# Optimization experiments

Hardware: AMD Instinct MI355X
Metric: run time of the kernel (lower is better)

Reference implementation:

```python
import jax, jax.numpy as jnp
import numpy as np

FEATURE_DIM = 512
DEPTH = 128
NUM_CLASSES = 1000


def setup_inputs() -> dict:
    key = jax.random.key(0)
    ks = jax.random.split(key, 9)
    s = 1.0 / np.sqrt(FEATURE_DIM)
    sd = 1.0 / np.sqrt(DEPTH)
    return {
        "x": jax.random.normal(ks[0], (8, 2048, FEATURE_DIM), dtype=jnp.float32),
        "Wq": jax.random.uniform(ks[1], (FEATURE_DIM, DEPTH), jnp.float32, -s, s),
        "bq": jax.random.uniform(ks[2], (DEPTH,), jnp.float32, -s, s),
        "Wk": jax.random.uniform(ks[3], (FEATURE_DIM, DEPTH), jnp.float32, -s, s),
        "bk": jax.random.uniform(ks[4], (DEPTH,), jnp.float32, -s, s),
        "Wv": jax.random.uniform(ks[5], (FEATURE_DIM, DEPTH), jnp.float32, -s, s),
        "bv": jax.random.uniform(ks[6], (DEPTH,), jnp.float32, -s, s),
        "Wl": jax.random.uniform(ks[7], (DEPTH, NUM_CLASSES), jnp.float32, -sd, sd),
        "bl": jax.random.uniform(ks[8], (NUM_CLASSES,), jnp.float32, -sd, sd),
    }


def reference(x, Wq, bq, Wk, bk, Wv, bv, Wl, bl):
    # q,k,v: [B,S,depth]
    q = jnp.einsum("bsf,fd->bsd", x, Wq) + bq
    k = jnp.einsum("bsf,fd->bsd", x, Wk) + bk
    v = jnp.einsum("bsf,fd->bsd", x, Wv) + bv
    # NOTE: original applies no 1/sqrt(depth) scaling
    logit = jnp.einsum("bqd,bkd->bqk", q, k)  # [B,S,S]
    attn = jax.nn.softmax(logit, axis=2)
    attn_out = jnp.einsum("bqk,bkd->bqd", attn, v)  # [B,S,depth]
    out = jnp.einsum("bsd,dc->bsc", attn_out, Wl) + bl  # [B,S,C]
    return out.mean(axis=1)  # [B,C]
```

## Files before the change

### kernel.cpp

```cpp
#include <hip/hip_runtime.h>
#include <stdint.h>

#define NB 8
#define SS 2048
#define FF 512
#define DD 128
#define CC 1000
#define KC 8
#define CHUNK (SS / KC)

typedef __attribute__((ext_vector_type(8))) short bf16x8;
typedef __attribute__((ext_vector_type(4))) float f32x4;

__device__ __forceinline__ short f2bf(float f) {
    uint32_t u;
    __builtin_memcpy(&u, &f, 4);
    u = (u + 0x7fffu + ((u >> 16) & 1u)) >> 16;
    return (short)u;
}
__device__ __forceinline__ float bf2f(short h) {
    uint32_t u = ((uint32_t)(uint16_t)h) << 16;
    float f;
    __builtin_memcpy(&f, &u, 4);
    return f;
}
__device__ __forceinline__ void async16(const void* g, void* l) {
    __builtin_amdgcn_global_load_lds(
        (const __attribute__((address_space(1))) uint32_t*)g,
        (__attribute__((address_space(3))) uint32_t*)l, 16, 0, 0);
}

__global__ void prep(const float* __restrict__ x,
                     const float* __restrict__ Wq, const float* __restrict__ Wk,
                     const float* __restrict__ Wv,
                     short* __restrict__ xb, short* __restrict__ Wt)
{
    int bx = blockIdx.x;
    if (bx < 4096) {
        int id = bx * 256 + threadIdx.x;
        const float4* src = (const float4*)x + id * 2;
        float4 a = src[0], b2 = src[1];
        bf16x8 o;
        o[0] = f2bf(a.x);  o[1] = f2bf(a.y);  o[2] = f2bf(a.z);  o[3] = f2bf(a.w);
        o[4] = f2bf(b2.x); o[5] = f2bf(b2.y); o[6] = f2bf(b2.z); o[7] = f2bf(b2.w);
        *(bf16x8*)(xb + id * 8) = o;
    } else {
        int id = (bx - 4096) * 256 + threadIdx.x;
        int w = id >> 16, rem = id & 65535;
        int n = rem >> 9, kx = rem & 511;
        const float* Wsrc = (w == 0) ? Wq : (w == 1) ? Wk : Wv;
        Wt[w * 65536 + n * 512 + kx] = f2bf(Wsrc[kx * 128 + n]);
    }
}

__global__ __launch_bounds__(256) void qkv_proj(
    const short* __restrict__ xb, const short* __restrict__ Wt,
    const float* __restrict__ bq, const float* __restrict__ bk, const float* __restrict__ bv,
    short* __restrict__ qo, short* __restrict__ ko, short* __restrict__ vto)
{
    __shared__ __align__(16) short As[128 * 64];
    __shared__ __align__(16) short Bs[128 * 64];

    const int m0   = blockIdx.x * 128;
    const int mat  = blockIdx.y;
    const int tid  = threadIdx.x;
    const int wave = tid >> 6, lane = tid & 63;
    const int quad = lane >> 4, l16 = lane & 15;
    const int wr = wave >> 1, wc = wave & 1;

    const short* Wm = Wt + mat * 65536;

    f32x4 acc[4][4];
    for (int i = 0; i < 4; i++)
        for (int j = 0; j < 4; j++) acc[i][j] = (f32x4){0.f, 0.f, 0.f, 0.f};

    const int sr = lane >> 3;
    const int sc = (lane & 7) ^ (sr & 7);

    for (int kk = 0; kk < 512; kk += 64) {
        __syncthreads();
        for (int i = 0; i < 4; i++) {
            int ins = wave * 4 + i;
            int r = ins * 8 + sr;
            async16(xb + (m0 + r) * 512 + kk + sc * 8, &As[ins * 512]);
            async16(Wm + r * 512 + kk + sc * 8,        &Bs[ins * 512]);
        }
        __syncthreads();

        for (int kc = 0; kc < 2; kc++) {
            bf16x8 af[4], bfr[4];
            for (int mt = 0; mt < 4; mt++) {
                int R = wr * 64 + mt * 16 + l16, cc = kc * 4 + quad;
                af[mt] = *(const bf16x8*)&As[(R * 8 + (cc ^ (R & 7))) * 8];
            }
            for (int nt = 0; nt < 4; nt++) {
                int R = wc * 64 + nt * 16 + l16, cc = kc * 4 + quad;
                bfr[nt] = *(const bf16x8*)&Bs[(R * 8 + (cc ^ (R & 7))) * 8];
            }
            for (int mt = 0; mt < 4; mt++)
                for (int nt = 0; nt < 4; nt++)
                    acc[mt][nt] = __builtin_amdgcn_mfma_f32_16x16x32_bf16(
                        af[mt], bfr[nt], acc[mt][nt], 0, 0, 0);
        }
    }

    const float* bias = (mat == 0) ? bq : (mat == 1) ? bk : bv;
    for (int mt = 0; mt < 4; mt++) {
        int grow_base = m0 + wr * 64 + mt * 16 + quad * 4;
        for (int nt = 0; nt < 4; nt++) {
            int col = wc * 64 + nt * 16 + l16;
            float bb = bias[col];
            for (int r = 0; r < 4; r++) {
                int grow = grow_base + r;
                short h = f2bf(acc[mt][nt][r] + bb);
                if (mat == 0)      qo[grow * 128 + col] = h;
                else if (mat == 1) ko[grow * 128 + col] = h;
                else {
                    int b_ = grow >> 11, si = grow & 2047;
                    vto[(b_ * 128 + col) * 2048 + si] = h;
                }
            }
        }
    }
}

__global__ __launch_bounds__(256) void flash_partial(
    const short* __restrict__ q, const short* __restrict__ k,
    const short* __restrict__ vt, short* __restrict__ O_part,
    float* __restrict__ l_part)
{
    __shared__ __align__(16) short ks[32 * 128];
    __shared__ __align__(16) short vs[128 * 32];
    __shared__ __align__(16) short ps[4 * 32 * 40];

    const int b   = blockIdx.y;
    const int q0  = blockIdx.x * 128;
    const int lq  = blockIdx.z;
    const int c0  = lq * CHUNK;
    const int tid  = threadIdx.x;
    const int wave = tid >> 6, lane = tid & 63;
    const int quad = lane >> 4, l16 = lane & 15;

    bf16x8 qf[2][4];
    for (int m = 0; m < 2; m++)
        for (int c = 0; c < 4; c++)
            qf[m][c] = *(const bf16x8*)(q + (b * 2048 + q0 + wave * 32 + m * 16 + l16) * 128
                                          + c * 32 + quad * 8);

    f32x4 O[2][8];
    for (int m = 0; m < 2; m++)
        for (int t = 0; t < 8; t++) O[m][t] = (f32x4){0.f, 0.f, 0.f, 0.f};
    float l_[2][4] = {{0.f,0.f,0.f,0.f},{0.f,0.f,0.f,0.f}};

    short* psw = ps + wave * (32 * 40);

    const int krl = lane >> 4;
    const int vrl = lane >> 2;
    const int vcl = (lane & 3) ^ ((lane >> 3) & 3);

    for (int s0 = c0; s0 < c0 + CHUNK; s0 += 32) {
        __syncthreads();
        for (int i2 = 0; i2 < 2; i2++) {
            int ik = wave * 2 + i2;
            int kr = 4 * ik + krl;
            int kc8 = (lane & 15) ^ (kr & 15);
            async16(k + (b * 2048 + s0 + kr) * 128 + kc8 * 8, &ks[ik * 512]);
            int vr = 16 * ik + vrl;
            async16(vt + (b * 128 + vr) * 2048 + s0 + vcl * 8, &vs[ik * 512]);
        }
        __syncthreads();

        f32x4 Sf[2][2];
        for (int m = 0; m < 2; m++)
            for (int ct = 0; ct < 2; ct++) Sf[m][ct] = (f32x4){0.f, 0.f, 0.f, 0.f};
        for (int ct = 0; ct < 2; ct++) {
            int R = ct * 16 + l16;
            for (int c = 0; c < 4; c++) {
                int cc = c * 4 + quad;
                bf16x8 kb = *(const bf16x8*)&ks[(R * 16 + (cc ^ l16)) * 8];
                for (int m = 0; m < 2; m++)
                    Sf[m][ct] = __builtin_amdgcn_mfma_f32_16x16x32_bf16(
                        qf[m][c], kb, Sf[m][ct], 0, 0, 0);
            }
        }

        for (int m = 0; m < 2; m++)
            for (int r = 0; r < 4; r++) {
                float p0 = __expf(Sf[m][0][r] - 10.0f);
                float p1 = __expf(Sf[m][1][r] - 10.0f);
                l_[m][r] += p0 + p1;
                psw[(m * 16 + quad * 4 + r) * 40 + l16]      = f2bf(p0);
                psw[(m * 16 + quad * 4 + r) * 40 + l16 + 16] = f2bf(p1);
            }
        __builtin_amdgcn_wave_barrier();
        __asm__ volatile("" ::: "memory");
        bf16x8 pf[2];
        for (int m = 0; m < 2; m++)
            pf[m] = *(const bf16x8*)&psw[(m * 16 + l16) * 40 + quad * 8];
        for (int t = 0; t < 8; t++) {
            int R = t * 16 + l16;
            bf16x8 vb = *(const bf16x8*)&vs[(R * 4 + (quad ^ ((l16 >> 1) & 3))) * 8];
            for (int m = 0; m < 2; m++)
                O[m][t] = __builtin_amdgcn_mfma_f32_16x16x32_bf16(pf[m], vb, O[m][t], 0, 0, 0);
        }
        __builtin_amdgcn_wave_barrier();
        __asm__ volatile("" ::: "memory");
    }

    const int base = (lq * 8 + b) * 2048;
    for (int m = 0; m < 2; m++)
        for (int r = 0; r < 4; r++) {
            float lv = l_[m][r];
            lv += __shfl_xor(lv, 1);
            lv += __shfl_xor(lv, 2);
            lv += __shfl_xor(lv, 4);
            lv += __shfl_xor(lv, 8);
            if (l16 == 0)
                l_part[base + q0 + wave * 32 + m * 16 + quad * 4 + r] = lv;
        }
    for (int m = 0; m < 2; m++)
        for (int t = 0; t < 8; t++)
            for (int r = 0; r < 4; r++) {
                int row = q0 + wave * 32 + m * 16 + quad * 4 + r;
                O_part[(size_t)(base + row) * 128 + t * 16 + l16] = f2bf(O[m][t][r]);
            }
}

__global__ void combine(const short* __restrict__ O_part, const float* __restrict__ l_part,
                        float* __restrict__ accum)
{
    const int b   = blockIdx.y;
    const int s0  = blockIdx.x * 64 + (threadIdx.x >> 7) * 32;
    const int col = threadIdx.x & 127;
    float sum = 0.f;
    for (int i = 0; i < 32; i++) {
        int s = s0 + i;
        float l = 0.f, o = 0.f;
        for (int kc = 0; kc < KC; kc++) {
            int base = (kc * 8 + b) * 2048 + s;
            l += l_part[base];
            o += bf2f(O_part[(size_t)base * 128 + col]);
        }
        sum += o / l;
    }
    atomicAdd(&accum[b * 128 + col], sum);
}

__global__ void final_proj(const float* __restrict__ accum, const float* __restrict__ Wl,
                           const float* __restrict__ bl, float* __restrict__ out)
{
    int id = blockIdx.x * 256 + threadIdx.x;
    if (id >= NB * CC) return;
    int b = id / CC, c = id % CC;
    float s = 0.f;
    for (int d = 0; d < 128; d++)
        s += accum[b * 128 + d] * Wl[d * 1000 + c];
    out[id] = s * (1.0f / 2048.0f) + bl[c];
}

extern "C" void kernel_launch(void* const* d_in, const int* in_sizes, int n_in,
                              void* d_out, int out_size, void* d_ws, size_t ws_size,
                              hipStream_t stream) {
    const float* x  = (const float*)d_in[0];
    const float* Wq = (const float*)d_in[1];
    const float* bq = (const float*)d_in[2];
    const float* Wk = (const float*)d_in[3];
    const float* bk = (const float*)d_in[4];
    const float* Wv = (const float*)d_in[5];
    const float* bv = (const float*)d_in[6];
    const float* Wl = (const float*)d_in[7];
    const float* bl = (const float*)d_in[8];
    float* out = (float*)d_out;

    char* ws = (char*)d_ws;
    short* qo     = (short*)(ws);
    short* ko     = (short*)(ws + 4194304);
    short* vto    = (short*)(ws + 8388608);
    short* xb     = (short*)(ws + 12582912);
    short* O_part = (short*)(ws + 12582912);
    short* Wt     = (short*)(ws + 46137344);
    float* l_part = (float*)(ws + 46530560);
    float* acc    = (float*)(ws + 47054848);

    hipMemsetAsync(acc, 0, NB * DD * sizeof(float), stream);
    prep<<<4864, 256, 0, stream>>>(x, Wq, Wk, Wv, xb, Wt);
    qkv_proj<<<dim3(128, 3), 256, 0, stream>>>(xb, Wt, bq, bk, bv, qo, ko, vto);
    flash_partial<<<dim3(16, 8, KC), 256, 0, stream>>>(qo, ko, vto, O_part, l_part);
    combine<<<dim3(32, 8), 256, 0, stream>>>(O_part, l_part, acc);
    final_proj<<<(NB * CC + 255) / 256, 256, 0, stream>>>(acc, Wl, bl, out);
}
```

Baseline: 170.9 us.

## Exploit mean over queries: compute column weights of attention instead of full PV

Because the output is averaged over queries, the attention output mean equals a weighted sum of V rows with weights being column sums of the normalized softmax matrix. The flash kernel is split into a pass computing row sums (attn_l), a second pass recomputing QK^T to accumulate normalized column weights (attn_w), and a small weighted-V reduction (wv). This removes the PV MFMAs, the partial O writes and the combine kernel, at the cost of computing QK^T and exp twice and adding atomics on the weight buffer.

```diff
diff --git a/kernel.cpp b/kernel.cpp
--- a/kernel.cpp
+++ b/kernel.cpp
@@ -124,19 +124,16 @@
     }
 }
 
-__global__ __launch_bounds__(256) void flash_partial(
+__global__ __launch_bounds__(256) void attn_l(
     const short* __restrict__ q, const short* __restrict__ k,
-    const short* __restrict__ vt, short* __restrict__ O_part,
     float* __restrict__ l_part)
 {
-    __shared__ __align__(16) short ks[32 * 128];
-    __shared__ __align__(16) short vs[128 * 32];
-    __shared__ __align__(16) short ps[4 * 32 * 40];
-
-    const int b   = blockIdx.y;
-    const int q0  = blockIdx.x * 128;
-    const int lq  = blockIdx.z;
-    const int c0  = lq * CHUNK;
+    __shared__ __align__(16) short ks[64 * 128];
+
+    const int b  = blockIdx.y;
+    const int q0 = blockIdx.x * 128;
+    const int lq = blockIdx.z;
+    const int c0 = lq * CHUNK;
     const int tid  = threadIdx.x;
     const int wave = tid >> 6, lane = tid & 63;
     const int quad = lane >> 4, l16 = lane & 15;
@@ -147,103 +144,140 @@
             qf[m][c] = *(const bf16x8*)(q + (b * 2048 + q0 + wave * 32 + m * 16 + l16) * 128
                                           + c * 32 + quad * 8);
 
-    f32x4 O[2][8];
-    for (int m = 0; m < 2; m++)
-        for (int t = 0; t < 8; t++) O[m][t] = (f32x4){0.f, 0.f, 0.f, 0.f};
-    float l_[2][4] = {{0.f,0.f,0.f,0.f},{0.f,0.f,0.f,0.f}};
-
-    short* psw = ps + wave * (32 * 40);
-
+    float lsum[2][4] = {{0.f,0.f,0.f,0.f},{0.f,0.f,0.f,0.f}};
     const int krl = lane >> 4;
-    const int vrl = lane >> 2;
-    const int vcl = (lane & 3) ^ ((lane >> 3) & 3);
-
-    for (int s0 = c0; s0 < c0 + CHUNK; s0 += 32) {
-        __syncthreads();
-        for (int i2 = 0; i2 < 2; i2++) {
-            int ik = wave * 2 + i2;
-            int kr = 4 * ik + krl;
+
+    for (int s0 = c0; s0 < c0 + CHUNK; s0 += 64) {
+        __syncthreads();
+        for (int i = 0; i < 4; i++) {
+            int ik = wave * 4 + i;
+            int kr = ik * 4 + krl;
             int kc8 = (lane & 15) ^ (kr & 15);
             async16(k + (b * 2048 + s0 + kr) * 128 + kc8 * 8, &ks[ik * 512]);
-            int vr = 16 * ik + vrl;
-            async16(vt + (b * 128 + vr) * 2048 + s0 + vcl * 8, &vs[ik * 512]);
-        }
-        __syncthreads();
-
-        f32x4 Sf[2][2];
-        for (int m = 0; m < 2; m++)
-            for (int ct = 0; ct < 2; ct++) Sf[m][ct] = (f32x4){0.f, 0.f, 0.f, 0.f};
-        for (int ct = 0; ct < 2; ct++) {
+        }
+        __syncthreads();
+
+        for (int ct = 0; ct < 4; ct++) {
+            f32x4 Sf[2];
+            Sf[0] = (f32x4){0.f,0.f,0.f,0.f};
+            Sf[1] = (f32x4){0.f,0.f,0.f,0.f};
             int R = ct * 16 + l16;
             for (int c = 0; c < 4; c++) {
                 int cc = c * 4 + quad;
                 bf16x8 kb = *(const bf16x8*)&ks[(R * 16 + (cc ^ l16)) * 8];
                 for (int m = 0; m < 2; m++)
-                    Sf[m][ct] = __builtin_amdgcn_mfma_f32_16x16x32_bf16(
-                        qf[m][c], kb, Sf[m][ct], 0, 0, 0);
-            }
-        }
-
-        for (int m = 0; m < 2; m++)
-            for (int r = 0; r < 4; r++) {
-                float p0 = __expf(Sf[m][0][r] - 10.0f);
-                float p1 = __expf(Sf[m][1][r] - 10.0f);
-                l_[m][r] += p0 + p1;
-                psw[(m * 16 + quad * 4 + r) * 40 + l16]      = f2bf(p0);
-                psw[(m * 16 + quad * 4 + r) * 40 + l16 + 16] = f2bf(p1);
-            }
-        __builtin_amdgcn_wave_barrier();
-        __asm__ volatile("" ::: "memory");
-        bf16x8 pf[2];
-        for (int m = 0; m < 2; m++)
-            pf[m] = *(const bf16x8*)&psw[(m * 16 + l16) * 40 + quad * 8];
-        for (int t = 0; t < 8; t++) {
-            int R = t * 16 + l16;
-            bf16x8 vb = *(const bf16x8*)&vs[(R * 4 + (quad ^ ((l16 >> 1) & 3))) * 8];
+                    Sf[m] = __builtin_amdgcn_mfma_f32_16x16x32_bf16(
+                        qf[m][c], kb, Sf[m], 0, 0, 0);
+            }
             for (int m = 0; m < 2; m++)
-                O[m][t] = __builtin_amdgcn_mfma_f32_16x16x32_bf16(pf[m], vb, O[m][t], 0, 0, 0);
-        }
-        __builtin_amdgcn_wave_barrier();
-        __asm__ volatile("" ::: "memory");
-    }
-
-    const int base = (lq * 8 + b) * 2048;
+                for (int r = 0; r < 4; r++)
+                    lsum[m][r] += __expf(Sf[m][r] - 10.0f);
+        }
+    }
+
     for (int m = 0; m < 2; m++)
         for (int r = 0; r < 4; r++) {
-            float lv = l_[m][r];
+            float lv = lsum[m][r];
             lv += __shfl_xor(lv, 1);
             lv += __shfl_xor(lv, 2);
             lv += __shfl_xor(lv, 4);
             lv += __shfl_xor(lv, 8);
             if (l16 == 0)
-                l_part[base + q0 + wave * 32 + m * 16 + quad * 4 + r] = lv;
-        }
+                l_part[(lq * 8 + b) * 2048 + q0 + wave * 32 + m * 16 + quad * 4 + r] = lv;
+        }
+}
+
+__global__ __launch_bounds__(256) void attn_w(
+    const short* __restrict__ q, const short* __restrict__ k,
+    const float* __restrict__ l_part, float* __restrict__ w)
+{
+    __shared__ __align__(16) short ks[64 * 128];
+    __shared__ float wl[4][256];
+
+    const int b  = blockIdx.y;
+    const int q0 = blockIdx.x * 128;
+    const int lq = blockIdx.z;
+    const int c0 = lq * CHUNK;
+    const int tid  = threadIdx.x;
+    const int wave = tid >> 6, lane = tid & 63;
+    const int quad = lane >> 4, l16 = lane & 15;
+
+    bf16x8 qf[2][4];
     for (int m = 0; m < 2; m++)
-        for (int t = 0; t < 8; t++)
-            for (int r = 0; r < 4; r++) {
-                int row = q0 + wave * 32 + m * 16 + quad * 4 + r;
-                O_part[(size_t)(base + row) * 128 + t * 16 + l16] = f2bf(O[m][t][r]);
-            }
-}
-
-__global__ void combine(const short* __restrict__ O_part, const float* __restrict__ l_part,
-                        float* __restrict__ accum)
-{
-    const int b   = blockIdx.y;
-    const int s0  = blockIdx.x * 64 + (threadIdx.x >> 7) * 32;
-    const int col = threadIdx.x & 127;
-    float sum = 0.f;
-    for (int i = 0; i < 32; i++) {
-        int s = s0 + i;
-        float l = 0.f, o = 0.f;
-        for (int kc = 0; kc < KC; kc++) {
-            int base = (kc * 8 + b) * 2048 + s;
-            l += l_part[base];
-            o += bf2f(O_part[(size_t)base * 128 + col]);
-        }
-        sum += o / l;
-    }
-    atomicAdd(&accum[b * 128 + col], sum);
+        for (int c = 0; c < 4; c++)
+            qf[m][c] = *(const bf16x8*)(q + (b * 2048 + q0 + wave * 32 + m * 16 + l16) * 128
+                                          + c * 32 + quad * 8);
+
+    float linv[2][4];
+    for (int m = 0; m < 2; m++)
+        for (int r = 0; r < 4; r++) {
+            int row = q0 + wave * 32 + m * 16 + quad * 4 + r;
+            float lt = 0.f;
+            for (int kc = 0; kc < KC; kc++) lt += l_part[(kc * 8 + b) * 2048 + row];
+            linv[m][r] = 1.0f / lt;
+        }
+
+    const int krl = lane >> 4;
+
+    for (int s0 = c0; s0 < c0 + CHUNK; s0 += 64) {
+        __syncthreads();
+        for (int i = 0; i < 4; i++) {
+            int ik = wave * 4 + i;
+            int kr = ik * 4 + krl;
+            int kc8 = (lane & 15) ^ (kr & 15);
+            async16(k + (b * 2048 + s0 + kr) * 128 + kc8 * 8, &ks[ik * 512]);
+        }
+        __syncthreads();
+
+        for (int ct = 0; ct < 4; ct++) {
+            f32x4 Sf[2];
+            Sf[0] = (f32x4){0.f,0.f,0.f,0.f};
+            Sf[1] = (f32x4){0.f,0.f,0.f,0.f};
+            int R = ct * 16 + l16;
+            for (int c = 0; c < 4; c++) {
+                int cc = c * 4 + quad;
+                bf16x8 kb = *(const bf16x8*)&ks[(R * 16 + (cc ^ l16)) * 8];
+                for (int m = 0; m < 2; m++)
+                    Sf[m] = __builtin_amdgcn_mfma_f32_16x16x32_bf16(
+                        qf[m][c], kb, Sf[m], 0, 0, 0);
+            }
+            float cs = 0.f;
+            for (int m = 0; m < 2; m++)
+                for (int r = 0; r < 4; r++)
+                    cs += __expf(Sf[m][r] - 10.0f) * linv[m][r];
+            cs += __shfl_xor(cs, 16);
+            cs += __shfl_xor(cs, 32);
+            if (quad == 0) wl[wave][(s0 - c0) + ct * 16 + l16] = cs;
+        }
+    }
+
+    __syncthreads();
+    {
+        float s = wl[0][tid] + wl[1][tid] + wl[2][tid] + wl[3][tid];
+        atomicAdd(&w[b * 2048 + c0 + tid], s);
+    }
+}
+
+__global__ void wv(const float* __restrict__ w, const short* __restrict__ vt,
+                   float* __restrict__ accum)
+{
+    const int b  = blockIdx.x;
+    const int dg = blockIdx.y;
+    const int tid = threadIdx.x;
+    const int d  = dg * 16 + (tid >> 4);
+    const int sr = (tid & 15) * 128;
+    const float* wb = w + b * 2048 + sr;
+    const short* vp = vt + (size_t)(b * 128 + d) * 2048 + sr;
+    float s = 0.f;
+    for (int i = 0; i < 128; i += 8) {
+        bf16x8 v8 = *(const bf16x8*)(vp + i);
+        for (int j = 0; j < 8; j++) s += wb[i + j] * bf2f(v8[j]);
+    }
+    s += __shfl_xor(s, 1);
+    s += __shfl_xor(s, 2);
+    s += __shfl_xor(s, 4);
+    s += __shfl_xor(s, 8);
+    if ((tid & 15) == 0) accum[b * 128 + d] = s;
 }
 
 __global__ void final_proj(const float* __restrict__ accum, const float* __restrict__ Wl,
@@ -277,15 +311,16 @@
     short* ko     = (short*)(ws + 4194304);
     short* vto    = (short*)(ws + 8388608);
     short* xb     = (short*)(ws + 12582912);
-    short* O_part = (short*)(ws + 12582912);
-    short* Wt     = (short*)(ws + 46137344);
-    float* l_part = (float*)(ws + 46530560);
-    float* acc    = (float*)(ws + 47054848);
-
-    hipMemsetAsync(acc, 0, NB * DD * sizeof(float), stream);
+    short* Wt     = (short*)(ws + 29360128);
+    float* l_part = (float*)(ws + 29753344);
+    float* wbuf   = (float*)(ws + 30277632);
+    float* acc    = (float*)(ws + 30343168);
+
+    hipMemsetAsync(wbuf, 0, (size_t)NB * SS * sizeof(float), stream);
     prep<<<4864, 256, 0, stream>>>(x, Wq, Wk, Wv, xb, Wt);
     qkv_proj<<<dim3(128, 3), 256, 0, stream>>>(xb, Wt, bq, bk, bv, qo, ko, vto);
-    flash_partial<<<dim3(16, 8, KC), 256, 0, stream>>>(qo, ko, vto, O_part, l_part);
-    combine<<<dim3(32, 8), 256, 0, stream>>>(O_part, l_part, acc);
+    attn_l<<<dim3(16, 8, KC), 256, 0, stream>>>(qo, ko, l_part);
+    attn_w<<<dim3(16, 8, KC), 256, 0, stream>>>(qo, ko, l_part, wbuf);
+    wv<<<dim3(8, 8), 256, 0, stream>>>(wbuf, vto, acc);
     final_proj<<<(NB * CC + 255) / 256, 256, 0, stream>>>(acc, Wl, bl, out);
 }
```

Result: faster. 160.8 us (-6.0%).
